# Kernel tuning notes

Measured on AMD Instinct MI355X. Metric: run time of the kernel, lower is better.

Reference implementation:

```python
import jax, jax.numpy as jnp
import numpy as np

D = 2048   # embed_dim
E = 128    # expand_ratio = head dim
H = D // E # num heads = 16
C = 64     # chunk size for the chunked linear-attention scan
EPS = 1e-6


def setup_inputs() -> dict:
    key = jax.random.key(0)
    ks = jax.random.split(key, 6)
    b, n = 2, 2048
    s = 0.02
    x = jax.random.normal(ks[0], (b, n, D), jnp.float32)
    Wq = (jax.random.normal(ks[1], (D, D), jnp.float32) * s)
    Wk = (jax.random.normal(ks[2], (D, D), jnp.float32) * s)
    Wv = (jax.random.normal(ks[3], (D, D), jnp.float32) * s)
    Wf = (jax.random.normal(ks[4], (D, H), jnp.float32) * s)
    Wo = (jax.random.normal(ks[5], (D, D), jnp.float32) * s)
    norm_w = jnp.ones((D,), jnp.float32)
    return {"x": x, "Wq": Wq, "Wk": Wk, "Wv": Wv, "Wf": Wf, "Wo": Wo, "norm_w": norm_w}


def _lightning_scalar_decay(q, k, v, ld):
    # q,k,v: [b,n,H,E], ld: [b,n,H] log decay per head per step.
    # Recurrence: S_t = exp(ld_t) * S_{t-1} + k_t^T v_t ; o_t = q_t @ S_t
    b, n, h, e = q.shape
    nc = n // C
    qc = q.reshape(b, nc, C, h, e)
    kc = k.reshape(b, nc, C, h, e)
    vc = v.reshape(b, nc, C, h, e)
    ldc = ld.reshape(b, nc, C, h)
    cum = jnp.cumsum(ldc, axis=2)          # inclusive within-chunk log decay [b,nc,C,h]
    tot = cum[:, :, -1, :]                 # [b,nc,h]

    # intra-chunk: scores[i,j] = (q_i . k_j) * exp(L_i - L_j), j <= i
    Lh = cum.transpose(0, 1, 3, 2)         # [b,nc,h,C]
    decay = jnp.exp(Lh[..., :, None] - Lh[..., None, :])  # [b,nc,h,C,C]
    mask = jnp.tril(jnp.ones((C, C), bool))
    scores = jnp.einsum('bmihe,bmjhe->bmhij', qc, kc) * decay
    scores = jnp.where(mask, scores, 0.0)
    o_intra = jnp.einsum('bmhij,bmjhe->bmihe', scores, vc)

    # inter-chunk: carried recurrent state S [b,h,e,e]
    def step(S, inp):
        q_c, k_c, v_c, cum_c, tot_c = inp  # [b,C,h,e],...,[b,C,h],[b,h]
        o = jnp.einsum('bihe,bhef->bihf', q_c * jnp.exp(cum_c)[..., None], S)
        kd = k_c * jnp.exp(tot_c[:, None, :] - cum_c)[..., None]
        S_new = S * jnp.exp(tot_c)[:, :, None, None] + jnp.einsum('bihe,bihf->bhef', kd, v_c)
        return S_new, o

    xs = (qc.transpose(1, 0, 2, 3, 4), kc.transpose(1, 0, 2, 3, 4),
          vc.transpose(1, 0, 2, 3, 4), cum.transpose(1, 0, 2, 3), tot.transpose(1, 0, 2))
    S0 = jnp.zeros((b, h, e, e), q.dtype)
    S_final, o_inter = jax.lax.scan(step, S0, xs)
    o_inter = o_inter.transpose(1, 0, 2, 3, 4)  # [b,nc,C,h,e]
    return (o_intra + o_inter).reshape(b, n, h * e), S_final


def reference(x, Wq, Wk, Wv, Wf, Wo, norm_w):
    b, n, d = x.shape
    q = jax.nn.silu(x @ Wq).reshape(b, n, H, E)
    k = jax.nn.silu(x @ Wk).reshape(b, n, H, E)
    v = (x @ Wv).reshape(b, n, H, E)
    ld = jax.nn.log_sigmoid(x @ Wf)  # [b,n,H]
    o, _ = _lightning_scalar_decay(q, k, v, ld)
    # RMSNorm over full embed dim
    o = o * jax.lax.rsqrt(jnp.mean(o * o, axis=-1, keepdims=True) + EPS) * norm_w
    return o @ Wo
```

## Files before the change

### kernel.cpp

```cpp
#include <hip/hip_runtime.h>
#include <hip/hip_bf16.h>
#include <stdint.h>

#define D_ 2048
#define E_ 128
#define H_ 16
#define NB_ 2
#define NSEQ_ 2048
#define NTOK_ 4096
#define NCH_ 32

typedef short bf16s;
typedef __attribute__((ext_vector_type(8))) short bf16x8;
typedef __attribute__((ext_vector_type(4))) float f32x4;

__device__ __forceinline__ short f2b(float f) {
  __hip_bfloat16 h = __float2bfloat16(f);
  return *reinterpret_cast<short*>(&h);
}
__device__ __forceinline__ float b2f(short s) {
  __hip_bfloat16 h;
  *reinterpret_cast<short*>(&h) = s;
  return __bfloat162float(h);
}

__device__ __forceinline__ void gload_lds16(const void* g, void* l) {
  __builtin_amdgcn_global_load_lds(
      (__attribute__((address_space(1))) void*)(const_cast<void*>(g)),
      (__attribute__((address_space(3))) void*)(l), 16, 0, 0);
}

__global__ __launch_bounds__(256)
void cvt_bf16(const float* __restrict__ x, bf16s* __restrict__ y) {
  const size_t i = (size_t)blockIdx.x * 256 + threadIdx.x;
  const float4 a = ((const float4*)x)[i * 2];
  const float4 b = ((const float4*)x)[i * 2 + 1];
  bf16x8 o;
  o[0] = f2b(a.x); o[1] = f2b(a.y); o[2] = f2b(a.z); o[3] = f2b(a.w);
  o[4] = f2b(b.x); o[5] = f2b(b.y); o[6] = f2b(b.z); o[7] = f2b(b.w);
  *(bf16x8*)&y[i * 8] = o;
}

__global__ __launch_bounds__(256)
void transpose_w(const float* __restrict__ Wq, const float* __restrict__ Wk,
                 const float* __restrict__ Wv, const float* __restrict__ Wo,
                 const float* __restrict__ nw, bf16s* __restrict__ WqT,
                 bf16s* __restrict__ WkT, bf16s* __restrict__ WvT,
                 bf16s* __restrict__ WoT) {
  const float* src; bf16s* dst;
  if (blockIdx.z == 0)      { src = Wq; dst = WqT; }
  else if (blockIdx.z == 1) { src = Wk; dst = WkT; }
  else if (blockIdx.z == 2) { src = Wv; dst = WvT; }
  else                      { src = Wo; dst = WoT; }
  __shared__ float tile[64][65];
  const int n0 = blockIdx.x * 64, k0 = blockIdx.y * 64;
  const int t = threadIdx.x;
  const int tr = t >> 6, tc = t & 63;
#pragma unroll
  for (int rr = 0; rr < 16; ++rr) {
    const int row = rr * 4 + tr;
    tile[row][tc] = src[(size_t)(k0 + row) * D_ + n0 + tc];
  }
  __syncthreads();
  const float wk = (blockIdx.z == 3) ? nw[k0 + tc] : 1.f;
#pragma unroll
  for (int rr = 0; rr < 16; ++rr) {
    const int row = rr * 4 + tr;
    dst[(size_t)(n0 + row) * D_ + k0 + tc] = f2b(tile[tc][row] * wk);
  }
}

__global__ __launch_bounds__(256)
void ld_gemm(const float* __restrict__ x, const float* __restrict__ Wf,
             float* __restrict__ ldb) {
  const int t = threadIdx.x;
  const int col = t & 15;
  const int tok = blockIdx.x * 16 + (t >> 4);
  const float4* xr = (const float4*)(x + (size_t)tok * D_);
  float s = 0.f;
#pragma unroll 4
  for (int kk = 0; kk < D_ / 4; ++kk) {
    const float4 xv = xr[kk];
    const int k4 = kk * 4;
    s += xv.x * Wf[(k4 + 0) * H_ + col];
    s += xv.y * Wf[(k4 + 1) * H_ + col];
    s += xv.z * Wf[(k4 + 2) * H_ + col];
    s += xv.w * Wf[(k4 + 3) * H_ + col];
  }
  const float m = fminf(s, 0.f);
  ldb[(size_t)tok * H_ + col] = m - log1pf(__expf(-fabsf(s)));
}

template <typename OT>
__device__ __forceinline__ void gemm_body(const bf16s* __restrict__ A,
                                          const bf16s* __restrict__ Bt,
                                          OT* __restrict__ Cm, int bm, int bn,
                                          int act, const float* __restrict__ rs) {
  constexpr int BK = 64;
  __shared__ bf16s As[128 * BK];
  __shared__ bf16s Bs[128 * BK];
  const int t = threadIdx.x;
  const int w = t >> 6, l = t & 63;
  const int wm = w >> 1, wn = w & 1;
  const int lr = l & 15, lk = l >> 4;
  const int sr8 = l >> 3, sc = l & 7;
  const int cs = sc ^ sr8;
  f32x4 acc[4][4] = {};

  const size_t abase = (size_t)(bm * 128) * D_;
  const size_t bbase = (size_t)(bn * 128) * D_;

  for (int k0 = 0; k0 < D_; k0 += BK) {
    __syncthreads();
#pragma unroll
    for (int j = 0; j < 4; ++j) {
      const int row = w * 32 + j * 8;
      gload_lds16(&A[abase + (size_t)(row + sr8) * D_ + k0 + cs * 8],
                  &As[row * BK]);
      gload_lds16(&Bt[bbase + (size_t)(row + sr8) * D_ + k0 + cs * 8],
                  &Bs[row * BK]);
    }
    __syncthreads();
    bf16x8 af[4][2], bfr[4][2];
#pragma unroll
    for (int tm = 0; tm < 4; ++tm) {
      const int row = wm * 64 + tm * 16 + lr;
#pragma unroll
      for (int ks = 0; ks < 2; ++ks)
        af[tm][ks] =
            *(const bf16x8*)&As[row * BK + ((ks * 4 + lk) ^ (row & 7)) * 8];
    }
#pragma unroll
    for (int tn = 0; tn < 4; ++tn) {
      const int row = wn * 64 + tn * 16 + lr;
#pragma unroll
      for (int ks = 0; ks < 2; ++ks)
        bfr[tn][ks] =
            *(const bf16x8*)&Bs[row * BK + ((ks * 4 + lk) ^ (row & 7)) * 8];
    }
#pragma unroll
    for (int ks = 0; ks < 2; ++ks)
#pragma unroll
      for (int tm = 0; tm < 4; ++tm)
#pragma unroll
        for (int tn = 0; tn < 4; ++tn)
          acc[tm][tn] = __builtin_amdgcn_mfma_f32_16x16x32_bf16(
              af[tm][ks], bfr[tn][ks], acc[tm][tn], 0, 0, 0);
  }

#pragma unroll
  for (int tm = 0; tm < 4; ++tm) {
    const int rowb = bm * 128 + wm * 64 + tm * 16 + lk * 4;
#pragma unroll
    for (int tn = 0; tn < 4; ++tn) {
      const int col = bn * 128 + wn * 64 + tn * 16 + lr;
#pragma unroll
      for (int r = 0; r < 4; ++r) {
        float vv = acc[tm][tn][r];
        if (act) vv = vv / (1.f + __expf(-vv));
        if constexpr (sizeof(OT) == 2) {
          Cm[(size_t)(rowb + r) * D_ + col] = f2b(vv);
        } else {
          vv *= rs[rowb + r];
          Cm[(size_t)(rowb + r) * D_ + col] = vv;
        }
      }
    }
  }
}

__global__ __launch_bounds__(256)
void gemm_qkv(const bf16s* __restrict__ xb, const bf16s* __restrict__ WqT,
              const bf16s* __restrict__ WkT, const bf16s* __restrict__ WvT,
              bf16s* __restrict__ qb, bf16s* __restrict__ kb,
              bf16s* __restrict__ vb) {
  const int orig = blockIdx.x;
  const int lin = (orig & 7) * 192 + (orig >> 3);
  const int bm = lin & 31;
  const int bnz = lin >> 5;
  const int z = bnz >> 4, bn = bnz & 15;
  const bf16s* Bt; bf16s* out; int act;
  if (z == 0)      { Bt = WqT; out = qb; act = 1; }
  else if (z == 1) { Bt = WkT; out = kb; act = 1; }
  else             { Bt = WvT; out = vb; act = 0; }
  gemm_body<bf16s>(xb, Bt, out, bm, bn, act, nullptr);
}

__global__ __launch_bounds__(256)
void gemm_out(const bf16s* __restrict__ A, const bf16s* __restrict__ Bt,
              const float* __restrict__ rs, float* __restrict__ out) {
  const int orig = blockIdx.x;
  const int lin = (orig & 7) * 64 + (orig >> 3);
  const int bm = lin & 31;
  const int bn = lin >> 5;
  gemm_body<float>(A, Bt, out, bm, bn, 0, rs);
}

__global__ __launch_bounds__(256)
void chunk_state(const bf16s* __restrict__ k, const bf16s* __restrict__ v,
                 const float* __restrict__ ldp, bf16s* __restrict__ Mbuf,
                 float* __restrict__ totb) {
  const int c = blockIdx.x, bh = blockIdx.y;
  const int b = bh >> 4, h = bh & 15;
  const int t = threadIdx.x;
  const int w = t >> 6, l = t & 63;
  const int lr = l & 15, lk = l >> 4;

  __shared__ bf16s Kt[64 * 128];
  __shared__ bf16s Vn[64 * 128];
  __shared__ bf16s KdT[128 * 64];
  __shared__ bf16s VtT[128 * 64];
  __shared__ float cumS[64];
  char* cKt = (char*)Kt; char* cVn = (char*)Vn;
  char* cKdT = (char*)KdT; char* cVtT = (char*)VtT;

  const size_t grow0 = (size_t)b * NSEQ_ + c * 64;
#pragma unroll
  for (int j = 0; j < 4; ++j) {
    const int lrow = w * 16 + j * 4 + (l >> 4);
    const int ck = (l & 15) ^ (lrow & 7);
    const size_t goff = (grow0 + lrow) * D_ + h * E_ + ck * 8;
    const int lbase = (w * 16 + j * 4) * 128;
    gload_lds16(&k[goff], &Kt[lbase]);
    gload_lds16(&v[goff], &Vn[lbase]);
  }
  if (w == 0) {
    float val = ldp[(grow0 + l) * H_ + h];
#pragma unroll
    for (int off = 1; off < 64; off <<= 1) {
      float pv = __shfl_up(val, off);
      if (l >= off) val += pv;
    }
    cumS[l] = val;
  }
  __syncthreads();
  const float tot = cumS[63];
  if (t == 0) totb[bh * NCH_ + c] = tot;

#pragma unroll
  for (int it = 0; it < 4; ++it) {
    const int task = t + it * 256;
    const int i = task >> 4, cx = task & 15;
    const int sb = i * 256 + ((cx * 16) ^ ((i & 7) << 4));
    bf16x8 vv = *(const bf16x8*)(cVn + sb);
    bf16x8 kk8 = *(const bf16x8*)(cKt + sb);
    const float sE = __expf(tot - cumS[i]);
#pragma unroll
    for (int jj = 0; jj < 8; ++jj) {
      const int e = cx * 8 + jj;
      const int db = e * 128 + ((i * 2) ^ ((e & 7) << 4));
      *(bf16s*)(cVtT + db) = vv[jj];
      *(bf16s*)(cKdT + db) = f2b(b2f(kk8[jj]) * sE);
    }
  }
  __syncthreads();

  const int wm = w >> 1, wn = w & 1;
  f32x4 acc[4][4] = {};
#pragma unroll
  for (int kk2 = 0; kk2 < 2; ++kk2) {
    const int cb = (kk2 * 32 + lk * 8) * 2;
    bf16x8 af[4], bfr[4];
#pragma unroll
    for (int tm = 0; tm < 4; ++tm) {
      const int fr = wm * 64 + tm * 16 + lr;
      af[tm] = *(const bf16x8*)(cVtT + fr * 128 + (cb ^ ((fr & 7) << 4)));
    }
#pragma unroll
    for (int tn = 0; tn < 4; ++tn) {
      const int er = wn * 64 + tn * 16 + lr;
      bfr[tn] = *(const bf16x8*)(cKdT + er * 128 + (cb ^ ((er & 7) << 4)));
    }
#pragma unroll
    for (int tm = 0; tm < 4; ++tm)
#pragma unroll
      for (int tn = 0; tn < 4; ++tn)
        acc[tm][tn] = __builtin_amdgcn_mfma_f32_16x16x32_bf16(
            af[tm], bfr[tn], acc[tm][tn], 0, 0, 0);
  }
  const size_t mb = (size_t)(bh * NCH_ + c) * 128 * 128;
#pragma unroll
  for (int tm = 0; tm < 4; ++tm) {
#pragma unroll
    for (int tn = 0; tn < 4; ++tn) {
#pragma unroll
      for (int r = 0; r < 4; ++r) {
        const int f = wm * 64 + tm * 16 + lk * 4 + r;
        const int e = wn * 64 + tn * 16 + lr;
        Mbuf[mb + f * 128 + e] = f2b(acc[tm][tn][r]);
      }
    }
  }
}

__global__ __launch_bounds__(256)
void state_scan(const bf16s* __restrict__ Mbuf, const float* __restrict__ totb,
                bf16s* __restrict__ Sbuf) {
  const int sl = blockIdx.x;
  const int bh = blockIdx.y;
  const int t = threadIdx.x;
  const int fr = sl * 16 + (t >> 4);
  const int e0 = (t & 15) * 8;
  const size_t base = ((size_t)(bh * NCH_) * 128 + fr) * 128 + e0;
  const size_t cstride = 128 * 128;
  __shared__ float tots[NCH_];
  if (t < NCH_) tots[t] = totb[bh * NCH_ + t];
  __syncthreads();
  float acc[8] = {};
  bf16x8 m0 = *(const bf16x8*)&Mbuf[base + 0 * cstride];
  bf16x8 m1 = *(const bf16x8*)&Mbuf[base + 1 * cstride];
  bf16x8 m2 = *(const bf16x8*)&Mbuf[base + 2 * cstride];
  bf16x8 m3 = *(const bf16x8*)&Mbuf[base + 3 * cstride];
#pragma unroll
  for (int c = 0; c < NCH_; ++c) {
    bf16x8 sv;
#pragma unroll
    for (int j = 0; j < 8; ++j) sv[j] = f2b(acc[j]);
    *(bf16x8*)&Sbuf[base + (size_t)c * cstride] = sv;
    const bf16x8 mc = ((c & 3) == 0) ? m0 : ((c & 3) == 1) ? m1
                     : ((c & 3) == 2) ? m2 : m3;
    const float dt = __expf(tots[c]);
#pragma unroll
    for (int j = 0; j < 8; ++j) acc[j] = acc[j] * dt + b2f(mc[j]);
    if (c + 4 < NCH_) {
      const bf16x8 mn = *(const bf16x8*)&Mbuf[base + (size_t)(c + 4) * cstride];
      if ((c & 3) == 0) m0 = mn;
      else if ((c & 3) == 1) m1 = mn;
      else if ((c & 3) == 2) m2 = mn;
      else m3 = mn;
    }
  }
}

__global__ __launch_bounds__(256)
void attn_out(const bf16s* __restrict__ q, const bf16s* __restrict__ k,
              const bf16s* __restrict__ v, const float* __restrict__ ldp,
              const bf16s* __restrict__ Sbuf, bf16s* __restrict__ o) {
  const int c = blockIdx.x, bh = blockIdx.y;
  const int b = bh >> 4, h = bh & 15;
  const int t = threadIdx.x;
  const int w = t >> 6, l = t & 63;
  const int lr = l & 15, lk = l >> 4;

  __shared__ bf16s Qt[64 * 128];
  __shared__ bf16s Kt[64 * 128];
  __shared__ bf16s Vn[64 * 128];
  __shared__ bf16s VtT[128 * 64];
  __shared__ bf16s Pm[64 * 64];
  __shared__ float cumS[64];
  char* cQt = (char*)Qt; char* cKt = (char*)Kt; char* cVn = (char*)Vn;
  char* cVtT = (char*)VtT; char* cPm = (char*)Pm;

  const size_t grow0 = (size_t)b * NSEQ_ + c * 64;
  const size_t sbase = (size_t)(bh * NCH_ + c) * 128 * 128;
  const bf16x8* Sp = (const bf16x8*)&Sbuf[sbase];
#pragma unroll
  for (int j = 0; j < 4; ++j) {
    const int lrow = w * 16 + j * 4 + (l >> 4);
    const int ck = (l & 15) ^ (lrow & 7);
    const size_t goff = (grow0 + lrow) * D_ + h * E_ + ck * 8;
    const int lbase = (w * 16 + j * 4) * 128;
    gload_lds16(&q[goff], &Qt[lbase]);
    gload_lds16(&k[goff], &Kt[lbase]);
    gload_lds16(&v[goff], &Vn[lbase]);
  }
  if (w == 0) {
    float val = ldp[(grow0 + l) * H_ + h];
#pragma unroll
    for (int off = 1; off < 64; off <<= 1) {
      float pv = __shfl_up(val, off);
      if (l >= off) val += pv;
    }
    cumS[l] = val;
  }
  __syncthreads();

#pragma unroll
  for (int it = 0; it < 4; ++it) {
    const int task = t + it * 256;
    const int i = task >> 4, cx = task & 15;
    const int sb = i * 256 + ((cx * 16) ^ ((i & 7) << 4));
    bf16x8 vv = *(const bf16x8*)(cVn + sb);
#pragma unroll
    for (int jj = 0; jj < 8; ++jj) {
      const int e = cx * 8 + jj;
      const int db = e * 128 + ((i * 2) ^ ((e & 7) << 4));
      *(bf16s*)(cVtT + db) = vv[jj];
    }
  }

  f32x4 accs[4] = {};
  f32x4 acco[8] = {};
#pragma unroll
  for (int kk = 0; kk < 4; ++kk) {
    const int cb = (kk * 32 + lk * 8) * 2;
    const int ar = w * 16 + lr;
    bf16x8 aq = *(const bf16x8*)(cQt + ar * 256 + (cb ^ ((ar & 7) << 4)));
#pragma unroll
    for (int tn = 0; tn < 4; ++tn) {
      const int br = tn * 16 + lr;
      bf16x8 bk = *(const bf16x8*)(cKt + br * 256 + (cb ^ ((br & 7) << 4)));
      accs[tn] = __builtin_amdgcn_mfma_f32_16x16x32_bf16(aq, bk, accs[tn], 0, 0, 0);
    }
#pragma unroll
    for (int tf = 0; tf < 8; ++tf) {
      bf16x8 bs = Sp[(tf * 16 + lr) * 16 + kk * 4 + lk];
      acco[tf] = __builtin_amdgcn_mfma_f32_16x16x32_bf16(aq, bs, acco[tf], 0, 0, 0);
    }
  }
#pragma unroll
  for (int r = 0; r < 4; ++r) {
    const float gI = __expf(cumS[w * 16 + lk * 4 + r]);
#pragma unroll
    for (int tf = 0; tf < 8; ++tf) acco[tf][r] *= gI;
  }
#pragma unroll
  for (int tn = 0; tn < 4; ++tn) {
    const int j = tn * 16 + lr;
    const float cj = cumS[j];
#pragma unroll
    for (int r = 0; r < 4; ++r) {
      const int i = w * 16 + lk * 4 + r;
      const float sv = (j <= i) ? accs[tn][r] * __expf(cumS[i] - cj) : 0.f;
      *(bf16s*)(cPm + i * 128 + ((j * 2) ^ ((i & 7) << 4))) = f2b(sv);
    }
  }
  __syncthreads();

#pragma unroll
  for (int kk2 = 0; kk2 < 2; ++kk2) {
    const int cb = (kk2 * 32 + lk * 8) * 2;
    const int pr = w * 16 + lr;
    bf16x8 ap = *(const bf16x8*)(cPm + pr * 128 + (cb ^ ((pr & 7) << 4)));
#pragma unroll
    for (int tf = 0; tf < 8; ++tf) {
      const int fr = tf * 16 + lr;
      bf16x8 bv = *(const bf16x8*)(cVtT + fr * 128 + (cb ^ ((fr & 7) << 4)));
      acco[tf] = __builtin_amdgcn_mfma_f32_16x16x32_bf16(ap, bv, acco[tf], 0, 0, 0);
    }
  }
#pragma unroll
  for (int tf = 0; tf < 8; ++tf) {
#pragma unroll
    for (int r = 0; r < 4; ++r) {
      const int i = w * 16 + lk * 4 + r;
      o[(grow0 + i) * D_ + h * E_ + tf * 16 + lr] = f2b(acco[tf][r]);
    }
  }
}

__global__ __launch_bounds__(256)
void rms_scale(const bf16s* __restrict__ o, float* __restrict__ sout) {
  const int tok = blockIdx.x;
  const int t = threadIdx.x;
  bf16x8 vv = *(const bf16x8*)&o[(size_t)tok * D_ + t * 8];
  float s = 0.f;
#pragma unroll
  for (int j = 0; j < 8; ++j) { const float f = b2f(vv[j]); s += f * f; }
#pragma unroll
  for (int off2 = 32; off2 > 0; off2 >>= 1) s += __shfl_down(s, off2);
  __shared__ float wsum[4];
  if ((t & 63) == 0) wsum[t >> 6] = s;
  __syncthreads();
  if (t == 0)
    sout[tok] = rsqrtf((wsum[0] + wsum[1] + wsum[2] + wsum[3]) * (1.f / D_) +
                       1e-6f);
}

extern "C" void kernel_launch(void* const* d_in, const int* in_sizes, int n_in,
                              void* d_out, int out_size, void* d_ws,
                              size_t ws_size, hipStream_t stream) {
  (void)in_sizes; (void)n_in; (void)out_size;
  const float* x  = (const float*)d_in[0];
  const float* Wq = (const float*)d_in[1];
  const float* Wk = (const float*)d_in[2];
  const float* Wv = (const float*)d_in[3];
  const float* Wf = (const float*)d_in[4];
  const float* Wo = (const float*)d_in[5];
  const float* nw = (const float*)d_in[6];
  float* out = (float*)d_out;

  char* ws = (char*)d_ws;
  const size_t MB = 1024 * 1024;
  bf16s* xb   = (bf16s*)(ws + 0);
  bf16s* WqT  = (bf16s*)(ws + 16 * MB);
  bf16s* WkT  = (bf16s*)(ws + 24 * MB);
  bf16s* WvT  = (bf16s*)(ws + 32 * MB);
  bf16s* Sbuf = (bf16s*)(ws + 0);
  float* totb = (float*)(ws + 32 * MB);
  bf16s* WoT  = (bf16s*)(ws + 40 * MB);
  bf16s* qb   = (bf16s*)(ws + 48 * MB);
  bf16s* kb   = (bf16s*)(ws + 64 * MB);
  bf16s* vb   = (bf16s*)(ws + 80 * MB);
  bf16s* ob   = (bf16s*)(ws + 96 * MB);
  bf16s* Mbuf = (bf16s*)(ws + 112 * MB);
  float* ldb  = (float*)(ws + 144 * MB);
  float* rsb  = (float*)(ws + 145 * MB);
  if (146 * MB > ws_size) return;

  cvt_bf16<<<NTOK_ * D_ / 8 / 256, 256, 0, stream>>>(x, xb);
  transpose_w<<<dim3(32, 32, 4), 256, 0, stream>>>(Wq, Wk, Wv, Wo, nw, WqT,
                                                   WkT, WvT, WoT);
  ld_gemm<<<NTOK_ / 16, 256, 0, stream>>>(x, Wf, ldb);
  gemm_qkv<<<1536, 256, 0, stream>>>(xb, WqT, WkT, WvT, qb, kb, vb);
  chunk_state<<<dim3(NCH_, NB_ * H_), 256, 0, stream>>>(kb, vb, ldb, Mbuf, totb);
  state_scan<<<dim3(8, NB_ * H_), 256, 0, stream>>>(Mbuf, totb, Sbuf);
  attn_out<<<dim3(NCH_, NB_ * H_), 256, 0, stream>>>(qb, kb, vb, ldb, Sbuf, ob);
  rms_scale<<<NTOK_, 256, 0, stream>>>(ob, rsb);
  gemm_out<<<512, 256, 0, stream>>>(ob, WoT, rsb, out);
}
```

Before: 312.7 us.

## Merge prep kernels and fuse RMS sum-of-squares into attention output

Combines the x conversion, weight transposes and log-decay projection into a single prep kernel that also zeroes the RMS accumulator. The separate rms_scale pass is removed: attn_out reduces per-row squared outputs with shuffles and atomically adds them per token, and gemm_out computes the rsqrt inline. This cuts two kernel launches and one full read of the attention output, at the cost of atomics and a sum of squares taken from fp32 accumulators rather than the bf16-rounded values.

```diff
diff --git a/kernel.cpp b/kernel.cpp
--- a/kernel.cpp
+++ b/kernel.cpp
@@ -31,64 +31,66 @@
 }
 
 __global__ __launch_bounds__(256)
-void cvt_bf16(const float* __restrict__ x, bf16s* __restrict__ y) {
-  const size_t i = (size_t)blockIdx.x * 256 + threadIdx.x;
-  const float4 a = ((const float4*)x)[i * 2];
-  const float4 b = ((const float4*)x)[i * 2 + 1];
-  bf16x8 o;
-  o[0] = f2b(a.x); o[1] = f2b(a.y); o[2] = f2b(a.z); o[3] = f2b(a.w);
-  o[4] = f2b(b.x); o[5] = f2b(b.y); o[6] = f2b(b.z); o[7] = f2b(b.w);
-  *(bf16x8*)&y[i * 8] = o;
-}
-
-__global__ __launch_bounds__(256)
-void transpose_w(const float* __restrict__ Wq, const float* __restrict__ Wk,
-                 const float* __restrict__ Wv, const float* __restrict__ Wo,
-                 const float* __restrict__ nw, bf16s* __restrict__ WqT,
-                 bf16s* __restrict__ WkT, bf16s* __restrict__ WvT,
-                 bf16s* __restrict__ WoT) {
-  const float* src; bf16s* dst;
-  if (blockIdx.z == 0)      { src = Wq; dst = WqT; }
-  else if (blockIdx.z == 1) { src = Wk; dst = WkT; }
-  else if (blockIdx.z == 2) { src = Wv; dst = WvT; }
-  else                      { src = Wo; dst = WoT; }
+void prep(const float* __restrict__ x, const float* __restrict__ Wq,
+          const float* __restrict__ Wk, const float* __restrict__ Wv,
+          const float* __restrict__ Wo, const float* __restrict__ Wf,
+          const float* __restrict__ nw, bf16s* __restrict__ xb,
+          bf16s* __restrict__ WqT, bf16s* __restrict__ WkT,
+          bf16s* __restrict__ WvT, bf16s* __restrict__ WoT,
+          float* __restrict__ ldb, float* __restrict__ rsb) {
   __shared__ float tile[64][65];
-  const int n0 = blockIdx.x * 64, k0 = blockIdx.y * 64;
+  const int bid = blockIdx.x;
   const int t = threadIdx.x;
-  const int tr = t >> 6, tc = t & 63;
-#pragma unroll
-  for (int rr = 0; rr < 16; ++rr) {
-    const int row = rr * 4 + tr;
-    tile[row][tc] = src[(size_t)(k0 + row) * D_ + n0 + tc];
-  }
-  __syncthreads();
-  const float wk = (blockIdx.z == 3) ? nw[k0 + tc] : 1.f;
-#pragma unroll
-  for (int rr = 0; rr < 16; ++rr) {
-    const int row = rr * 4 + tr;
-    dst[(size_t)(n0 + row) * D_ + k0 + tc] = f2b(tile[tc][row] * wk);
-  }
-}
-
-__global__ __launch_bounds__(256)
-void ld_gemm(const float* __restrict__ x, const float* __restrict__ Wf,
-             float* __restrict__ ldb) {
-  const int t = threadIdx.x;
-  const int col = t & 15;
-  const int tok = blockIdx.x * 16 + (t >> 4);
-  const float4* xr = (const float4*)(x + (size_t)tok * D_);
-  float s = 0.f;
+  if (bid < 4096) {
+    const size_t i = (size_t)bid * 256 + t;
+    const float4 a = ((const float4*)x)[i * 2];
+    const float4 b = ((const float4*)x)[i * 2 + 1];
+    bf16x8 o;
+    o[0] = f2b(a.x); o[1] = f2b(a.y); o[2] = f2b(a.z); o[3] = f2b(a.w);
+    o[4] = f2b(b.x); o[5] = f2b(b.y); o[6] = f2b(b.z); o[7] = f2b(b.w);
+    *(bf16x8*)&xb[i * 8] = o;
+  } else if (bid < 8192) {
+    const int tid = bid - 4096;
+    const int z = tid >> 10;
+    const int rem = tid & 1023;
+    const int n0 = (rem & 31) * 64, k0 = (rem >> 5) * 64;
+    const float* src; bf16s* dst;
+    if (z == 0)      { src = Wq; dst = WqT; }
+    else if (z == 1) { src = Wk; dst = WkT; }
+    else if (z == 2) { src = Wv; dst = WvT; }
+    else             { src = Wo; dst = WoT; }
+    const int tr = t >> 6, tc = t & 63;
+#pragma unroll
+    for (int rr = 0; rr < 16; ++rr) {
+      const int row = rr * 4 + tr;
+      tile[row][tc] = src[(size_t)(k0 + row) * D_ + n0 + tc];
+    }
+    __syncthreads();
+    const float wk = (z == 3) ? nw[k0 + tc] : 1.f;
+#pragma unroll
+    for (int rr = 0; rr < 16; ++rr) {
+      const int row = rr * 4 + tr;
+      dst[(size_t)(n0 + row) * D_ + k0 + tc] = f2b(tile[tc][row] * wk);
+    }
+  } else {
+    const int blk = bid - 8192;
+    if (t < 16) rsb[blk * 16 + t] = 0.f;
+    const int col = t & 15;
+    const int tok = blk * 16 + (t >> 4);
+    const float4* xr = (const float4*)(x + (size_t)tok * D_);
+    float s = 0.f;
 #pragma unroll 4
-  for (int kk = 0; kk < D_ / 4; ++kk) {
-    const float4 xv = xr[kk];
-    const int k4 = kk * 4;
-    s += xv.x * Wf[(k4 + 0) * H_ + col];
-    s += xv.y * Wf[(k4 + 1) * H_ + col];
-    s += xv.z * Wf[(k4 + 2) * H_ + col];
-    s += xv.w * Wf[(k4 + 3) * H_ + col];
-  }
-  const float m = fminf(s, 0.f);
-  ldb[(size_t)tok * H_ + col] = m - log1pf(__expf(-fabsf(s)));
+    for (int kk = 0; kk < D_ / 4; ++kk) {
+      const float4 xv = xr[kk];
+      const int k4 = kk * 4;
+      s += xv.x * Wf[(k4 + 0) * H_ + col];
+      s += xv.y * Wf[(k4 + 1) * H_ + col];
+      s += xv.z * Wf[(k4 + 2) * H_ + col];
+      s += xv.w * Wf[(k4 + 3) * H_ + col];
+    }
+    const float m = fminf(s, 0.f);
+    ldb[(size_t)tok * H_ + col] = m - log1pf(__expf(-fabsf(s)));
+  }
 }
 
 template <typename OT>
@@ -161,7 +163,7 @@
         if constexpr (sizeof(OT) == 2) {
           Cm[(size_t)(rowb + r) * D_ + col] = f2b(vv);
         } else {
-          vv *= rs[rowb + r];
+          vv *= rsqrtf(rs[rowb + r] * (1.f / D_) + 1e-6f);
           Cm[(size_t)(rowb + r) * D_ + col] = vv;
         }
       }
@@ -335,7 +337,8 @@
 __global__ __launch_bounds__(256)
 void attn_out(const bf16s* __restrict__ q, const bf16s* __restrict__ k,
               const bf16s* __restrict__ v, const float* __restrict__ ldp,
-              const bf16s* __restrict__ Sbuf, bf16s* __restrict__ o) {
+              const bf16s* __restrict__ Sbuf, bf16s* __restrict__ o,
+              float* __restrict__ rsb) {
   const int c = blockIdx.x, bh = blockIdx.y;
   const int b = bh >> 4, h = bh & 15;
   const int t = threadIdx.x;
@@ -439,6 +442,21 @@
       acco[tf] = __builtin_amdgcn_mfma_f32_16x16x32_bf16(ap, bv, acco[tf], 0, 0, 0);
     }
   }
+  float ps[4];
+#pragma unroll
+  for (int r = 0; r < 4; ++r) {
+    float s = 0.f;
+#pragma unroll
+    for (int tf = 0; tf < 8; ++tf) s += acco[tf][r] * acco[tf][r];
+#pragma unroll
+    for (int off = 1; off < 16; off <<= 1) s += __shfl_xor(s, off);
+    ps[r] = s;
+  }
+  if (lr == 0) {
+#pragma unroll
+    for (int r = 0; r < 4; ++r)
+      atomicAdd(&rsb[grow0 + w * 16 + lk * 4 + r], ps[r]);
+  }
 #pragma unroll
   for (int tf = 0; tf < 8; ++tf) {
 #pragma unroll
@@ -447,24 +465,6 @@
       o[(grow0 + i) * D_ + h * E_ + tf * 16 + lr] = f2b(acco[tf][r]);
     }
   }
-}
-
-__global__ __launch_bounds__(256)
-void rms_scale(const bf16s* __restrict__ o, float* __restrict__ sout) {
-  const int tok = blockIdx.x;
-  const int t = threadIdx.x;
-  bf16x8 vv = *(const bf16x8*)&o[(size_t)tok * D_ + t * 8];
-  float s = 0.f;
-#pragma unroll
-  for (int j = 0; j < 8; ++j) { const float f = b2f(vv[j]); s += f * f; }
-#pragma unroll
-  for (int off2 = 32; off2 > 0; off2 >>= 1) s += __shfl_down(s, off2);
-  __shared__ float wsum[4];
-  if ((t & 63) == 0) wsum[t >> 6] = s;
-  __syncthreads();
-  if (t == 0)
-    sout[tok] = rsqrtf((wsum[0] + wsum[1] + wsum[2] + wsum[3]) * (1.f / D_) +
-                       1e-6f);
 }
 
 extern "C" void kernel_launch(void* const* d_in, const int* in_sizes, int n_in,
@@ -498,14 +498,12 @@
   float* rsb  = (float*)(ws + 145 * MB);
   if (146 * MB > ws_size) return;
 
-  cvt_bf16<<<NTOK_ * D_ / 8 / 256, 256, 0, stream>>>(x, xb);
-  transpose_w<<<dim3(32, 32, 4), 256, 0, stream>>>(Wq, Wk, Wv, Wo, nw, WqT,
-                                                   WkT, WvT, WoT);
-  ld_gemm<<<NTOK_ / 16, 256, 0, stream>>>(x, Wf, ldb);
+  prep<<<8448, 256, 0, stream>>>(x, Wq, Wk, Wv, Wo, Wf, nw, xb, WqT, WkT, WvT,
+                                 WoT, ldb, rsb);
   gemm_qkv<<<1536, 256, 0, stream>>>(xb, WqT, WkT, WvT, qb, kb, vb);
   chunk_state<<<dim3(NCH_, NB_ * H_), 256, 0, stream>>>(kb, vb, ldb, Mbuf, totb);
   state_scan<<<dim3(8, NB_ * H_), 256, 0, stream>>>(Mbuf, totb, Sbuf);
-  attn_out<<<dim3(NCH_, NB_ * H_), 256, 0, stream>>>(qb, kb, vb, ldb, Sbuf, ob);
-  rms_scale<<<NTOK_, 256, 0, stream>>>(ob, rsb);
+  attn_out<<<dim3(NCH_, NB_ * H_), 256, 0, stream>>>(qb, kb, vb, ldb, Sbuf, ob,
+                                                     rsb);
   gemm_out<<<512, 256, 0, stream>>>(ob, WoT, rsb, out);
 }
```

Measured after the change: 328.8 us. 1.05x slower.

## Halve GEMM K-tile to 32 with new LDS swizzle and raise occupancy hint

Applied to the files above, without the earlier changes.

The shared GEMM body now stages 32-wide K slices instead of 64, which halves LDS use per block. Because each row is now only four 16-byte chunks, the load mapping and XOR swizzle are rebuilt around that width. Both GEMM kernels declare launch bounds of 256 threads with 4 blocks per CU, so more blocks can be resident to hide memory latency. In exchange there are twice as many K iterations and barriers per tile, each with less MFMA work between syncs, and the register cap may cause spills.

```diff
diff --git a/kernel.cpp b/kernel.cpp
--- a/kernel.cpp
+++ b/kernel.cpp
@@ -96,15 +96,14 @@
                                           const bf16s* __restrict__ Bt,
                                           OT* __restrict__ Cm, int bm, int bn,
                                           int act, const float* __restrict__ rs) {
-  constexpr int BK = 64;
+  constexpr int BK = 32;
   __shared__ bf16s As[128 * BK];
   __shared__ bf16s Bs[128 * BK];
   const int t = threadIdx.x;
   const int w = t >> 6, l = t & 63;
   const int wm = w >> 1, wn = w & 1;
   const int lr = l & 15, lk = l >> 4;
-  const int sr8 = l >> 3, sc = l & 7;
-  const int cs = sc ^ sr8;
+  const int sr4 = l >> 2, sc = l & 3;
   f32x4 acc[4][4] = {};
 
   const size_t abase = (size_t)(bm * 128) * D_;
@@ -113,39 +112,31 @@
   for (int k0 = 0; k0 < D_; k0 += BK) {
     __syncthreads();
 #pragma unroll
-    for (int j = 0; j < 4; ++j) {
-      const int row = w * 32 + j * 8;
-      gload_lds16(&A[abase + (size_t)(row + sr8) * D_ + k0 + cs * 8],
-                  &As[row * BK]);
-      gload_lds16(&Bt[bbase + (size_t)(row + sr8) * D_ + k0 + cs * 8],
-                  &Bs[row * BK]);
+    for (int j = 0; j < 2; ++j) {
+      const int row0 = j * 64 + w * 16;
+      const int row = row0 + sr4;
+      const int cs = sc ^ ((row >> 1) & 3);
+      gload_lds16(&A[abase + (size_t)row * D_ + k0 + cs * 8], &As[row0 * BK]);
+      gload_lds16(&Bt[bbase + (size_t)row * D_ + k0 + cs * 8], &Bs[row0 * BK]);
     }
     __syncthreads();
-    bf16x8 af[4][2], bfr[4][2];
+    bf16x8 af[4], bfr[4];
 #pragma unroll
     for (int tm = 0; tm < 4; ++tm) {
       const int row = wm * 64 + tm * 16 + lr;
-#pragma unroll
-      for (int ks = 0; ks < 2; ++ks)
-        af[tm][ks] =
-            *(const bf16x8*)&As[row * BK + ((ks * 4 + lk) ^ (row & 7)) * 8];
+      af[tm] = *(const bf16x8*)&As[row * BK + (lk ^ ((row >> 1) & 3)) * 8];
     }
 #pragma unroll
     for (int tn = 0; tn < 4; ++tn) {
       const int row = wn * 64 + tn * 16 + lr;
-#pragma unroll
-      for (int ks = 0; ks < 2; ++ks)
-        bfr[tn][ks] =
-            *(const bf16x8*)&Bs[row * BK + ((ks * 4 + lk) ^ (row & 7)) * 8];
-    }
-#pragma unroll
-    for (int ks = 0; ks < 2; ++ks)
-#pragma unroll
-      for (int tm = 0; tm < 4; ++tm)
-#pragma unroll
-        for (int tn = 0; tn < 4; ++tn)
-          acc[tm][tn] = __builtin_amdgcn_mfma_f32_16x16x32_bf16(
-              af[tm][ks], bfr[tn][ks], acc[tm][tn], 0, 0, 0);
+      bfr[tn] = *(const bf16x8*)&Bs[row * BK + (lk ^ ((row >> 1) & 3)) * 8];
+    }
+#pragma unroll
+    for (int tm = 0; tm < 4; ++tm)
+#pragma unroll
+      for (int tn = 0; tn < 4; ++tn)
+        acc[tm][tn] = __builtin_amdgcn_mfma_f32_16x16x32_bf16(
+            af[tm], bfr[tn], acc[tm][tn], 0, 0, 0);
   }
 
 #pragma unroll
@@ -169,7 +160,7 @@
   }
 }
 
-__global__ __launch_bounds__(256)
+__global__ __launch_bounds__(256, 4)
 void gemm_qkv(const bf16s* __restrict__ xb, const bf16s* __restrict__ WqT,
               const bf16s* __restrict__ WkT, const bf16s* __restrict__ WvT,
               bf16s* __restrict__ qb, bf16s* __restrict__ kb,
@@ -186,7 +177,7 @@
   gemm_body<bf16s>(xb, Bt, out, bm, bn, act, nullptr);
 }
 
-__global__ __launch_bounds__(256)
+__global__ __launch_bounds__(256, 4)
 void gemm_out(const bf16s* __restrict__ A, const bf16s* __restrict__ Bt,
               const float* __restrict__ rs, float* __restrict__ out) {
   const int orig = blockIdx.x;
```

Result: no change. 317.9 us (+1.7%).

## Replace QKV GEMM with 256x256 tile, 8-wave, double-buffered pipelined kernel

Applied to the files above, without the earlier changes.

The fused QKV projection GEMM now uses a 512-thread kernel with 256x256 output tiles and double-buffered LDS staged in quarter-tile pieces. Direct global-to-LDS loads are interleaved with MFMA phases under explicit vmcnt/lgkmcnt waits, barriers and s_setprio hints. The aim is to raise data reuse per tile and hide global memory latency behind MFMA work. The cost is 128 KB of LDS per block and 384 blocks, so tail effects and occupancy could limit the benefit. The output GEMM is left as the simpler 128x128 kernel.

```diff
diff --git a/kernel.cpp b/kernel.cpp
--- a/kernel.cpp
+++ b/kernel.cpp
@@ -28,6 +28,17 @@
   __builtin_amdgcn_global_load_lds(
       (__attribute__((address_space(1))) void*)(const_cast<void*>(g)),
       (__attribute__((address_space(3))) void*)(l), 16, 0, 0);
+}
+
+template <int N>
+__device__ __forceinline__ void wait_vmcnt() {
+  if constexpr (N == 0)      asm volatile("s_waitcnt vmcnt(0)" ::: "memory");
+  else if constexpr (N == 6) asm volatile("s_waitcnt vmcnt(6)" ::: "memory");
+  else static_assert(N == 0, "unsupported vmcnt");
+}
+__device__ __forceinline__ void lgkm0_fence() {
+  asm volatile("s_waitcnt lgkmcnt(0)" ::: "memory");
+  __builtin_amdgcn_sched_barrier(0);
 }
 
 __global__ __launch_bounds__(256)
@@ -91,11 +102,157 @@
   ldb[(size_t)tok * H_ + col] = m - log1pf(__expf(-fabsf(s)));
 }
 
-template <typename OT>
-__device__ __forceinline__ void gemm_body(const bf16s* __restrict__ A,
-                                          const bf16s* __restrict__ Bt,
-                                          OT* __restrict__ Cm, int bm, int bn,
-                                          int act, const float* __restrict__ rs) {
+__global__ __launch_bounds__(512, 2)
+void gemm_qkv8p(const bf16s* __restrict__ xb, const bf16s* __restrict__ WqT,
+                const bf16s* __restrict__ WkT, const bf16s* __restrict__ WvT,
+                bf16s* __restrict__ qb, bf16s* __restrict__ kb,
+                bf16s* __restrict__ vb) {
+  const int bn = blockIdx.x, bm = blockIdx.y, z = blockIdx.z;
+  const bf16s* Bt; bf16s* outp; int act;
+  if (z == 0)      { Bt = WqT; outp = qb; act = 1; }
+  else if (z == 1) { Bt = WkT; outp = kb; act = 1; }
+  else             { Bt = WvT; outp = vb; act = 0; }
+
+  __shared__ bf16s As[2 * 256 * 64];
+  __shared__ bf16s Bs[2 * 256 * 64];
+  const int t = threadIdx.x;
+  const int w = t >> 6, l = t & 63;
+  const int wm = w >> 2, wn = w & 3;
+  const int lr = l & 15, lk = l >> 4;
+
+  const size_t abase = (size_t)(bm * 256) * D_;
+  const size_t bbase = (size_t)(bn * 256) * D_;
+
+  f32x4 acc[8][4] = {};
+
+  auto stageHT = [&](int m, int part) {
+    const int slot = m & 1;
+    const int k0 = m * 64;
+    const int rowoff = (part >> 1) * 128;
+    const bool isB = part & 1;
+    const bf16s* g = isB ? Bt : xb;
+    const size_t gb = (isB ? bbase : abase) + (size_t)rowoff * D_ + k0;
+    bf16s* lb = (isB ? Bs : As) + slot * (256 * 64) + rowoff * 64;
+#pragma unroll
+    for (int rr = 0; rr < 2; ++rr) {
+      const int r = rr * 64 + (t >> 3);
+      const int cs = (t & 7) ^ (r & 7);
+      gload_lds16(&g[gb + (size_t)r * D_ + cs * 8], &lb[rr * 4096 + w * 512]);
+    }
+  };
+  auto ldA = [&](int slot, int fm, int ks) -> bf16x8 {
+    const int row = fm * 32 + wm * 16 + lr;
+    return *(const bf16x8*)&As[slot * (256 * 64) + row * 64 +
+                               (((ks << 2) + lk) ^ (row & 7)) * 8];
+  };
+  auto ldB = [&](int slot, int fn, int ks) -> bf16x8 {
+    const int row = fn * 64 + wn * 16 + lr;
+    return *(const bf16x8*)&Bs[slot * (256 * 64) + row * 64 +
+                               (((ks << 2) + lk) ^ (row & 7)) * 8];
+  };
+
+  stageHT(0, 0); stageHT(0, 1); stageHT(0, 2); stageHT(0, 3);
+  stageHT(1, 0); stageHT(1, 1); stageHT(1, 2);
+  wait_vmcnt<6>();
+  __builtin_amdgcn_s_barrier();
+
+  bf16x8 af[4][2], bf0[2][2], bf1[2][2];
+  for (int j = 0; j < 32; ++j) {
+    const int s = j & 1;
+#pragma unroll
+    for (int fm = 0; fm < 4; ++fm)
+#pragma unroll
+      for (int ks = 0; ks < 2; ++ks) af[fm][ks] = ldA(s, fm, ks);
+#pragma unroll
+    for (int fn = 0; fn < 2; ++fn)
+#pragma unroll
+      for (int ks = 0; ks < 2; ++ks) bf0[fn][ks] = ldB(s, fn, ks);
+    if (j <= 30) stageHT(j + 1, 3);
+    __builtin_amdgcn_s_barrier();
+    lgkm0_fence();
+    __builtin_amdgcn_s_setprio(1);
+#pragma unroll
+    for (int fm = 0; fm < 4; ++fm)
+#pragma unroll
+      for (int fn = 0; fn < 2; ++fn)
+#pragma unroll
+        for (int ks = 0; ks < 2; ++ks)
+          acc[fm][fn] = __builtin_amdgcn_mfma_f32_16x16x32_bf16(
+              af[fm][ks], bf0[fn][ks], acc[fm][fn], 0, 0, 0);
+    __builtin_amdgcn_s_setprio(0);
+    __builtin_amdgcn_s_barrier();
+#pragma unroll
+    for (int fn = 0; fn < 2; ++fn)
+#pragma unroll
+      for (int ks = 0; ks < 2; ++ks) bf1[fn][ks] = ldB(s, fn + 2, ks);
+    if (j <= 29) stageHT(j + 2, 0);
+    __builtin_amdgcn_s_barrier();
+    lgkm0_fence();
+    __builtin_amdgcn_s_setprio(1);
+#pragma unroll
+    for (int fm = 0; fm < 4; ++fm)
+#pragma unroll
+      for (int fn = 0; fn < 2; ++fn)
+#pragma unroll
+        for (int ks = 0; ks < 2; ++ks)
+          acc[fm][fn + 2] = __builtin_amdgcn_mfma_f32_16x16x32_bf16(
+              af[fm][ks], bf1[fn][ks], acc[fm][fn + 2], 0, 0, 0);
+    __builtin_amdgcn_s_setprio(0);
+    __builtin_amdgcn_s_barrier();
+#pragma unroll
+    for (int fm = 0; fm < 4; ++fm)
+#pragma unroll
+      for (int ks = 0; ks < 2; ++ks) af[fm][ks] = ldA(s, fm + 4, ks);
+    if (j <= 29) stageHT(j + 2, 1);
+    __builtin_amdgcn_s_barrier();
+    lgkm0_fence();
+    __builtin_amdgcn_s_setprio(1);
+#pragma unroll
+    for (int fm = 0; fm < 4; ++fm)
+#pragma unroll
+      for (int fn = 0; fn < 2; ++fn)
+#pragma unroll
+        for (int ks = 0; ks < 2; ++ks)
+          acc[fm + 4][fn + 2] = __builtin_amdgcn_mfma_f32_16x16x32_bf16(
+              af[fm][ks], bf1[fn][ks], acc[fm + 4][fn + 2], 0, 0, 0);
+    __builtin_amdgcn_s_setprio(0);
+    __builtin_amdgcn_s_barrier();
+    if (j <= 29) stageHT(j + 2, 2);
+    __builtin_amdgcn_s_setprio(1);
+#pragma unroll
+    for (int fm = 0; fm < 4; ++fm)
+#pragma unroll
+      for (int fn = 0; fn < 2; ++fn)
+#pragma unroll
+        for (int ks = 0; ks < 2; ++ks)
+          acc[fm + 4][fn] = __builtin_amdgcn_mfma_f32_16x16x32_bf16(
+              af[fm][ks], bf0[fn][ks], acc[fm + 4][fn], 0, 0, 0);
+    __builtin_amdgcn_s_setprio(0);
+    if (j <= 29)      wait_vmcnt<6>();
+    else if (j == 30) wait_vmcnt<0>();
+    __builtin_amdgcn_s_barrier();
+  }
+
+#pragma unroll
+  for (int fm = 0; fm < 8; ++fm) {
+    const int row = bm * 256 + fm * 32 + wm * 16 + lk * 4;
+#pragma unroll
+    for (int fn = 0; fn < 4; ++fn) {
+      const int col = bn * 256 + fn * 64 + wn * 16 + lr;
+#pragma unroll
+      for (int r = 0; r < 4; ++r) {
+        float vv = acc[fm][fn][r];
+        if (act) vv = vv / (1.f + __expf(-vv));
+        outp[(size_t)(row + r) * D_ + col] = f2b(vv);
+      }
+    }
+  }
+}
+
+__device__ __forceinline__ void gemm_body128(const bf16s* __restrict__ A,
+                                             const bf16s* __restrict__ Bt,
+                                             float* __restrict__ Cm, int bm,
+                                             int bn, const float* __restrict__ rs) {
   constexpr int BK = 64;
   __shared__ bf16s As[128 * BK];
   __shared__ bf16s Bs[128 * BK];
@@ -156,34 +313,11 @@
       const int col = bn * 128 + wn * 64 + tn * 16 + lr;
 #pragma unroll
       for (int r = 0; r < 4; ++r) {
-        float vv = acc[tm][tn][r];
-        if (act) vv = vv / (1.f + __expf(-vv));
-        if constexpr (sizeof(OT) == 2) {
-          Cm[(size_t)(rowb + r) * D_ + col] = f2b(vv);
-        } else {
-          vv *= rs[rowb + r];
-          Cm[(size_t)(rowb + r) * D_ + col] = vv;
-        }
+        float vv = acc[tm][tn][r] * rs[rowb + r];
+        Cm[(size_t)(rowb + r) * D_ + col] = vv;
       }
     }
   }
-}
-
-__global__ __launch_bounds__(256)
-void gemm_qkv(const bf16s* __restrict__ xb, const bf16s* __restrict__ WqT,
-              const bf16s* __restrict__ WkT, const bf16s* __restrict__ WvT,
-              bf16s* __restrict__ qb, bf16s* __restrict__ kb,
-              bf16s* __restrict__ vb) {
-  const int orig = blockIdx.x;
-  const int lin = (orig & 7) * 192 + (orig >> 3);
-  const int bm = lin & 31;
-  const int bnz = lin >> 5;
-  const int z = bnz >> 4, bn = bnz & 15;
-  const bf16s* Bt; bf16s* out; int act;
-  if (z == 0)      { Bt = WqT; out = qb; act = 1; }
-  else if (z == 1) { Bt = WkT; out = kb; act = 1; }
-  else             { Bt = WvT; out = vb; act = 0; }
-  gemm_body<bf16s>(xb, Bt, out, bm, bn, act, nullptr);
 }
 
 __global__ __launch_bounds__(256)
@@ -193,7 +327,7 @@
   const int lin = (orig & 7) * 64 + (orig >> 3);
   const int bm = lin & 31;
   const int bn = lin >> 5;
-  gemm_body<float>(A, Bt, out, bm, bn, 0, rs);
+  gemm_body128(A, Bt, out, bm, bn, rs);
 }
 
 __global__ __launch_bounds__(256)
@@ -502,7 +636,7 @@
   transpose_w<<<dim3(32, 32, 4), 256, 0, stream>>>(Wq, Wk, Wv, Wo, nw, WqT,
                                                    WkT, WvT, WoT);
   ld_gemm<<<NTOK_ / 16, 256, 0, stream>>>(x, Wf, ldb);
-  gemm_qkv<<<1536, 256, 0, stream>>>(xb, WqT, WkT, WvT, qb, kb, vb);
+  gemm_qkv8p<<<dim3(8, 16, 3), 512, 0, stream>>>(xb, WqT, WkT, WvT, qb, kb, vb);
   chunk_state<<<dim3(NCH_, NB_ * H_), 256, 0, stream>>>(kb, vb, ldb, Mbuf, totb);
   state_scan<<<dim3(8, NB_ * H_), 256, 0, stream>>>(Mbuf, totb, Sbuf);
   attn_out<<<dim3(NCH_, NB_ * H_), 256, 0, stream>>>(qb, kb, vb, ldb, Sbuf, ob);
```

Measured after the change: 299.3 us. -4.3%, faster.
